# Kernel tuning notes

Hardware: AMD Instinct MI355X
Metric: run time of the kernel (lower is better)

## Reference

```python
import jax, jax.numpy as jnp
import numpy as np

N, D, F, H, DH, R = 50000, 16, 256, 8, 32, 20
HOP_NUM, TOP_K, ALPHA, NEG_SLOPE = 10, 5, 0.1, 0.2
FF_HID = 4 * F


def _ln(x, g, b, eps=1e-5):
    m = x.mean(-1, keepdims=True)
    v = ((x - m) ** 2).mean(-1, keepdims=True)
    return (x - m) / jnp.sqrt(v + eps) * g + b


def setup_inputs() -> dict:
    key = jax.random.key(0)
    ks = jax.random.split(key, 16)
    s = 0.02
    inp = {
        'ent_feat': jax.random.normal(ks[0], (N, F), jnp.float32),
        'rel_feat': jax.random.normal(ks[1], (R, F), jnp.float32),
        'W_head': jax.random.normal(ks[2], (F, H * DH), jnp.float32) * s,
        'W_tail': jax.random.normal(ks[3], (F, H * DH), jnp.float32) * s,
        'W_ent': jax.random.normal(ks[4], (F, H * DH), jnp.float32) * s,
        'W_rel': jax.random.normal(ks[5], (F, H * DH), jnp.float32) * s,
        'attn_h': jax.random.normal(ks[6], (H, DH), jnp.float32) * s,
        'attn_t': jax.random.normal(ks[7], (H, DH), jnp.float32) * s,
        'attn_r': jax.random.normal(ks[8], (H, DH), jnp.float32) * s,
        'ln_ent_g': jnp.ones((F,), jnp.float32), 'ln_ent_b': jnp.zeros((F,), jnp.float32),
        'ln_rel_g': jnp.ones((F,), jnp.float32), 'ln_rel_b': jnp.zeros((F,), jnp.float32),
        'ln_ff_g': jnp.ones((F,), jnp.float32), 'ln_ff_b': jnp.zeros((F,), jnp.float32),
        'ffn_W1': jax.random.normal(ks[9], (F, FF_HID), jnp.float32) * s,
        'ffn_b1': jnp.zeros((FF_HID,), jnp.float32),
        'ffn_W2': jax.random.normal(ks[10], (FF_HID, F), jnp.float32) * s,
        'ffn_b2': jnp.zeros((F,), jnp.float32),
        'src': jax.random.randint(ks[11], (N, D), 0, N, jnp.int32),
        'rid': jax.random.randint(ks[12], (N, D), 0, R, jnp.int32),
    }
    return inp


def reference(ent_feat, rel_feat, W_head, W_tail, W_ent, W_rel,
              attn_h, attn_t, attn_r,
              ln_ent_g, ln_ent_b, ln_rel_g, ln_rel_b, ln_ff_g, ln_ff_b,
              ffn_W1, ffn_b1, ffn_W2, ffn_b2, src, rid):
    # --- projections (dropout = 0 at eval) ---
    x = _ln(ent_feat, ln_ent_g, ln_ent_b)                    # [N,F]
    fh = (x @ W_head).reshape(N, H, DH)
    ftl = (x @ W_tail).reshape(N, H, DH)
    fe = (x @ W_ent).reshape(N, H, DH)                       # 'ft' messages
    r = _ln(rel_feat, ln_rel_g, ln_rel_b)
    fr = (r @ W_rel).reshape(R, H, DH)
    # --- per-node / per-relation attention logits ---
    eh = (fh * attn_h).sum(-1)                               # [N,H]
    et = (ftl * attn_t).sum(-1)                              # [N,H]
    er = (fr * attn_r).sum(-1)                               # [R,H]
    # edges: row i = incoming edges of dst node i, sources src[i,:]
    e = eh[src] + et[:, None, :] + er[rid]                   # [N,D,H]
    e = jnp.where(e > 0, e, NEG_SLOPE * e)                   # LeakyReLU
    # --- edge_softmax over incoming edges of each dst node ---
    a = jax.nn.softmax(e, axis=1)                            # [N,D,H]
    # --- top-k sparsification + renormalization ---
    a_t = a.transpose(0, 2, 1)                               # [N,H,D]
    topv, _ = jax.lax.top_k(a_t, TOP_K)                      # [N,H,K]
    kth = topv[..., TOP_K - 1]                               # [N,H]
    top_sum = topv.sum(-1)                                   # [N,H]
    a_n = jnp.where(a_t >= kth[..., None], a_t, 0.0) / top_sum[..., None]  # [N,H,D]
    # --- PPR diffusion: feat <- (1-a) * A @ feat + a * feat0 ---
    feat0 = fe

    def step(feat, _):
        m = feat[src]                                        # [N,D,H,DH]
        agg = jnp.einsum('ndhk,nhd->nhk', m, a_n)            # [N,H,DH]
        return (1.0 - ALPHA) * agg + ALPHA * feat0, None

    feat, _ = jax.lax.scan(step, feat0, None, length=HOP_NUM)
    # --- residual (Identity since in==out) + FFN block ---
    rst = feat + ent_feat.reshape(N, H, DH)
    rst = rst.reshape(N, F)
    y = _ln(rst, ln_ff_g, ln_ff_b)
    ff = jax.nn.relu(y @ ffn_W1 + ffn_b1) @ ffn_W2 + ffn_b2
    return ff + rst
```

## Files before the change

kernel.cpp:

```cpp
#include <hip/hip_runtime.h>

#define NN   50000
#define DD   16
#define FFE  256
#define HH   8
#define DHH  32
#define RR   20
#define HOPN 10

typedef unsigned short u16;
typedef unsigned int   u32;
typedef __attribute__((ext_vector_type(8))) short  short8;
typedef __attribute__((ext_vector_type(4))) float  floatx4;

__device__ __forceinline__ float b2f(u16 u){ return __uint_as_float(((u32)u)<<16); }
__device__ __forceinline__ u16 f2b(float f){
  u32 x = __float_as_uint(f);
  u32 r = (x + 0x7fffu + ((x>>16)&1u)) >> 16;
  return (u16)r;
}

__global__ __launch_bounds__(256) void castw_kernel(
    const float* __restrict__ We, const float* __restrict__ W1,
    const float* __restrict__ W2,
    u16* __restrict__ Wet, u16* __restrict__ W1t, u16* __restrict__ W2t)
{
  int tid = blockIdx.x*256 + threadIdx.x;
  if (tid < 256*256) {
    int k = tid >> 8, n = tid & 255;
    Wet[n*256 + k] = f2b(We[tid]);
  } else if (tid < 256*256 + 256*1024) {
    int s = tid - 65536;
    int k = s >> 10, n = s & 1023;
    W1t[n*256 + k] = f2b(W1[s]);
  } else if (tid < 589824) {
    int s = tid - 327680;
    int k = s >> 8, n = s & 255;
    W2t[n*1024 + k] = f2b(W2[s]);
  }
}

__global__ __launch_bounds__(256) void prep_kernel(
    const float* __restrict__ rel_feat,
    const float* __restrict__ W_head, const float* __restrict__ W_tail,
    const float* __restrict__ W_rel,
    const float* __restrict__ attn_h, const float* __restrict__ attn_t,
    const float* __restrict__ attn_r,
    const float* __restrict__ lng, const float* __restrict__ lnb,
    double* __restrict__ Wc, double* __restrict__ er)
{
  int t = threadIdx.x;
  if (blockIdx.x == RR) {
    for (int h = 0; h < HH; h++) {
      double sh = 0.0, st = 0.0;
      #pragma unroll
      for (int c = 0; c < DHH; c++) {
        int j = h*DHH + c;
        sh += (double)W_head[t*FFE + j] * (double)attn_h[j];
        st += (double)W_tail[t*FFE + j] * (double)attn_t[j];
      }
      Wc[t*16 + h]     = sh;
      Wc[t*16 + 8 + h] = st;
    }
    return;
  }
  int r = blockIdx.x;
  __shared__ double red[8];
  __shared__ double rln[256];
  double v = (double)rel_feat[r*FFE + t];
  double s = v, q = v*v;
  #pragma unroll
  for (int o = 32; o; o >>= 1) { s += __shfl_xor(s, o, 64); q += __shfl_xor(q, o, 64); }
  if ((t & 63) == 0) { red[t>>6] = s; red[4 + (t>>6)] = q; }
  __syncthreads();
  double stot = red[0]+red[1]+red[2]+red[3];
  double qtot = red[4]+red[5]+red[6]+red[7];
  double mean = stot * (1.0/256.0);
  double var  = qtot * (1.0/256.0) - mean*mean;
  double rstd = 1.0 / sqrt(var + 1e-5);
  rln[t] = (v - mean) * rstd * (double)lng[t] + (double)lnb[t];
  __syncthreads();
  double acc = 0.0;
  for (int k = 0; k < 256; k++) acc += rln[k] * (double)W_rel[k*FFE + t];
  double p = acc * (double)attn_r[t];
  #pragma unroll
  for (int o = 16; o; o >>= 1) p += __shfl_down(p, o, 32);
  if ((t & 31) == 0) er[r*HH + (t>>5)] = p;
}

__global__ __launch_bounds__(256) void logits_kernel(
    const float* __restrict__ ent,
    const float* __restrict__ lng, const float* __restrict__ lnb,
    const double* __restrict__ Wc,
    u16* __restrict__ xb, double* __restrict__ eh, double* __restrict__ et)
{
  int tid = threadIdx.x;
  int w = tid >> 6, l = tid & 63;
  int rowA = blockIdx.x*8 + w*2;
  int rowB = rowA + 1;
  float gg[4], bbv[4];
  #pragma unroll
  for (int j = 0; j < 4; j++) { gg[j] = lng[l + 64*j]; bbv[j] = lnb[l + 64*j]; }
  double xA[4], xB[4];
  #pragma unroll
  for (int j = 0; j < 4; j++) xA[j] = (double)ent[(size_t)rowA*FFE + l + 64*j];
  #pragma unroll
  for (int j = 0; j < 4; j++) xB[j] = (double)ent[(size_t)rowB*FFE + l + 64*j];
  double sA = xA[0]+xA[1]+xA[2]+xA[3];
  double sB = xB[0]+xB[1]+xB[2]+xB[3];
  double qA = xA[0]*xA[0]+xA[1]*xA[1]+xA[2]*xA[2]+xA[3]*xA[3];
  double qB = xB[0]*xB[0]+xB[1]*xB[1]+xB[2]*xB[2]+xB[3]*xB[3];
  #pragma unroll
  for (int o = 32; o; o >>= 1) {
    sA += __shfl_xor(sA, o, 64); qA += __shfl_xor(qA, o, 64);
    sB += __shfl_xor(sB, o, 64); qB += __shfl_xor(qB, o, 64);
  }
  double mA = sA * (1.0/256.0), mB = sB * (1.0/256.0);
  double vA = qA * (1.0/256.0) - mA*mA, vB = qB * (1.0/256.0) - mB*mB;
  double rsA = 1.0 / sqrt(vA + 1e-5), rsB = 1.0 / sqrt(vB + 1e-5);
  #pragma unroll
  for (int j = 0; j < 4; j++) {
    double yA = (xA[j]-mA)*rsA*(double)gg[j] + (double)bbv[j];
    double yB = (xB[j]-mB)*rsB*(double)gg[j] + (double)bbv[j];
    xA[j] = yA; xB[j] = yB;
    xb[(size_t)rowA*FFE + l + 64*j] = f2b((float)yA);
    xb[(size_t)rowB*FFE + l + 64*j] = f2b((float)yB);
  }
  double accA[16], accB[16];
  #pragma unroll
  for (int o = 0; o < 16; o++) { accA[o] = 0.0; accB[o] = 0.0; }
  #pragma unroll
  for (int j = 0; j < 4; j++) {
    int k = l + 64*j;
    const double2* wp = (const double2*)(Wc + (size_t)k*16);
    double wv[16];
    #pragma unroll
    for (int u = 0; u < 8; u++) { double2 tv = wp[u]; wv[2*u] = tv.x; wv[2*u+1] = tv.y; }
    #pragma unroll
    for (int o = 0; o < 16; o++) {
      accA[o] = fma(xA[j], wv[o], accA[o]);
      accB[o] = fma(xB[j], wv[o], accB[o]);
    }
  }
  #pragma unroll
  for (int o = 0; o < 16; o++) {
    #pragma unroll
    for (int off = 32; off; off >>= 1) {
      accA[o] += __shfl_xor(accA[o], off, 64);
      accB[o] += __shfl_xor(accB[o], off, 64);
    }
  }
  #pragma unroll
  for (int o = 0; o < 16; o++) {
    if (l == o) {
      if (o < 8) eh[(size_t)rowA*HH + o] = accA[o];
      else       et[(size_t)rowA*HH + (o-8)] = accA[o];
    }
    if (l == 16 + o) {
      if (o < 8) eh[(size_t)rowB*HH + o] = accB[o];
      else       et[(size_t)rowB*HH + (o-8)] = accB[o];
    }
  }
}

template<int EPI>
__global__ __launch_bounds__(256) void gemm_kernel(
    const u16* __restrict__ A, const u16* __restrict__ B,
    const float* __restrict__ bias,
    const u16* __restrict__ feat, const float* __restrict__ ent,
    u16* __restrict__ Obf, float* __restrict__ Of,
    int M, int N, int K)
{
  __shared__ u16 As[128][40];
  __shared__ u16 Bs[128][40];
  int t = threadIdx.x;
  int i0 = blockIdx.x * 128;
  int n0 = blockIdx.y * 128;
  int w = t >> 6, l = t & 63;
  int cr = t >> 2;
  int cc = (t & 3) * 8;
  int ga0 = min(i0 + cr, M-1);
  int ga1 = min(i0 + cr + 64, M-1);
  int gb0 = n0 + cr;
  int gb1 = n0 + cr + 64;
  floatx4 acc[2][8];
  #pragma unroll
  for (int mt = 0; mt < 2; mt++)
    #pragma unroll
    for (int nt = 0; nt < 8; nt++) acc[mt][nt] = (floatx4){0.f,0.f,0.f,0.f};
  int ln = l & 15, lq = (l >> 4) * 8;
  for (int k0 = 0; k0 < K; k0 += 32) {
    __syncthreads();
    *(uint4*)&As[cr][cc]      = *(const uint4*)&A[(size_t)ga0*K + k0 + cc];
    *(uint4*)&As[cr+64][cc]   = *(const uint4*)&A[(size_t)ga1*K + k0 + cc];
    *(uint4*)&Bs[cr][cc]      = *(const uint4*)&B[(size_t)gb0*K + k0 + cc];
    *(uint4*)&Bs[cr+64][cc]   = *(const uint4*)&B[(size_t)gb1*K + k0 + cc];
    __syncthreads();
    short8 bfr[8];
    #pragma unroll
    for (int nt = 0; nt < 8; nt++) bfr[nt] = *(const short8*)&Bs[nt*16 + ln][lq];
    #pragma unroll
    for (int mt = 0; mt < 2; mt++) {
      short8 afr = *(const short8*)&As[w*32 + mt*16 + ln][lq];
      #pragma unroll
      for (int nt = 0; nt < 8; nt++)
        acc[mt][nt] = __builtin_amdgcn_mfma_f32_16x16x32_bf16(afr, bfr[nt], acc[mt][nt], 0, 0, 0);
    }
  }
  int lr = (l >> 4) * 4;
  #pragma unroll
  for (int mt = 0; mt < 2; mt++) {
    #pragma unroll
    for (int nt = 0; nt < 8; nt++) {
      int col = n0 + nt*16 + ln;
      #pragma unroll
      for (int r = 0; r < 4; r++) {
        int row = i0 + w*32 + mt*16 + lr + r;
        if (row < M) {
          float v = acc[mt][nt][r];
          if (EPI == 0) {
            Obf[(size_t)row*N + col] = f2b(v);
          } else if (EPI == 1) {
            v += bias[col];
            Obf[(size_t)row*N + col] = f2b(v > 0.f ? v : 0.f);
          } else {
            v += bias[col] + b2f(feat[(size_t)row*FFE + col]) + ent[(size_t)row*FFE + col];
            Of[(size_t)row*N + col] = v;
          }
        }
      }
    }
  }
}

__global__ __launch_bounds__(256) void edge_kernel(
    const int* __restrict__ src, const int* __restrict__ rid,
    const double* __restrict__ eh, const double* __restrict__ et,
    const double* __restrict__ er,
    int* __restrict__ idx6, float* __restrict__ w6)
{
  int tid = blockIdx.x*256 + threadIdx.x;
  if (tid >= NN*HH) return;
  int i = tid >> 3, h = tid & 7;
  double bet = et[tid];
  double e[16]; int sj[16];
  #pragma unroll
  for (int d = 0; d < 16; d++) {
    int s = src[i*DD + d];
    int rv = rid[i*DD + d];
    sj[d] = s;
    double v = eh[s*HH + h] + bet + er[rv*HH + h];
    e[d] = (v > 0.0) ? v : 0.2 * v;
  }
  u32 mask = 0; double vs[5]; int js[5];
  #pragma unroll
  for (int k = 0; k < 5; k++) {
    double best = -1e300; int bj = 0, bd = 0;
    #pragma unroll
    for (int d = 0; d < 16; d++) {
      bool c = (((mask>>d)&1u) == 0u) && (e[d] > best);
      if (c) { best = e[d]; bj = sj[d]; bd = d; }
    }
    mask |= (1u << bd); vs[k] = best; js[k] = bj;
  }
  double kth = vs[4];
  int j6 = 0; bool f6 = false;
  #pragma unroll
  for (int d = 0; d < 16; d++) {
    if ((((mask>>d)&1u) == 0u) && (e[d] == kth) && !f6) { j6 = sj[d]; f6 = true; }
  }
  float m0 = (float)vs[0];
  float ex[5], ssum = 0.f;
  #pragma unroll
  for (int k = 0; k < 5; k++) { ex[k] = __expf((float)vs[k] - m0); ssum += ex[k]; }
  float inv = 0.9f / ssum;
  long base = (long)tid * 6;
  #pragma unroll
  for (int k = 0; k < 5; k++) { idx6[base+k] = js[k]; w6[base+k] = ex[k]*inv; }
  idx6[base+5] = j6; w6[base+5] = f6 ? ex[4]*inv : 0.f;
}

__global__ __launch_bounds__(256) void diff_kernel(
    const u16* __restrict__ fold, const u16* __restrict__ fe,
    const int* __restrict__ idx6, const float* __restrict__ w6,
    u16* __restrict__ fnew)
{
  int tid = threadIdx.x;
  int i = blockIdx.x*2 + (tid >> 7);
  int t2 = tid & 127;
  int h = t2 >> 4, c2 = t2 & 15;
  const u32* fold32 = (const u32*)fold;
  const u32* fe32   = (const u32*)fe;
  u32* fnew32 = (u32*)fnew;
  long eb = ((long)i*HH + h) * 6;
  u32 fv = fe32[(size_t)i*128 + t2];
  float acc0 = 0.1f * b2f((u16)(fv & 0xffff));
  float acc1 = 0.1f * b2f((u16)(fv >> 16));
  #pragma unroll
  for (int k = 0; k < 5; k++) {
    int j = idx6[eb + k];
    float w = w6[eb + k];
    u32 v = fold32[(size_t)j*128 + h*16 + c2];
    acc0 += w * b2f((u16)(v & 0xffff));
    acc1 += w * b2f((u16)(v >> 16));
  }
  float w5 = w6[eb + 5];
  if (w5 != 0.f) {
    int j = idx6[eb + 5];
    u32 v = fold32[(size_t)j*128 + h*16 + c2];
    acc0 += w5 * b2f((u16)(v & 0xffff));
    acc1 += w5 * b2f((u16)(v >> 16));
  }
  fnew32[(size_t)i*128 + t2] = (u32)f2b(acc0) | ((u32)f2b(acc1) << 16);
}

__global__ __launch_bounds__(256) void ln_ff_kernel(
    const u16* __restrict__ feat, const float* __restrict__ ent,
    const float* __restrict__ g, const float* __restrict__ b,
    u16* __restrict__ y)
{
  int w = threadIdx.x >> 6, l = threadIdx.x & 63;
  int row = blockIdx.x*4 + w;
  float4 e4 = *(const float4*)&ent[row*FFE + l*4];
  ushort4 fv = *(const ushort4*)&feat[row*FFE + l*4];
  float v0 = b2f(fv.x)+e4.x, v1 = b2f(fv.y)+e4.y;
  float v2 = b2f(fv.z)+e4.z, v3 = b2f(fv.w)+e4.w;
  float s = v0+v1+v2+v3;
  float q = v0*v0 + v1*v1 + v2*v2 + v3*v3;
  #pragma unroll
  for (int o = 32; o; o >>= 1) { s += __shfl_xor(s, o, 64); q += __shfl_xor(q, o, 64); }
  float mean = s * (1.f/256.f);
  float var  = q * (1.f/256.f) - mean*mean;
  float rstd = rsqrtf(var + 1e-5f);
  float4 g4 = *(const float4*)&g[l*4];
  float4 b4 = *(const float4*)&b[l*4];
  ushort4 o4;
  o4.x = f2b((v0-mean)*rstd*g4.x + b4.x);
  o4.y = f2b((v1-mean)*rstd*g4.y + b4.y);
  o4.z = f2b((v2-mean)*rstd*g4.z + b4.z);
  o4.w = f2b((v3-mean)*rstd*g4.w + b4.w);
  *(ushort4*)&y[row*FFE + l*4] = o4;
}

extern "C" void kernel_launch(void* const* d_in, const int* in_sizes, int n_in,
                              void* d_out, int out_size, void* d_ws, size_t ws_size,
                              hipStream_t stream)
{
  const float* ent      = (const float*)d_in[0];
  const float* rel      = (const float*)d_in[1];
  const float* W_head   = (const float*)d_in[2];
  const float* W_tail   = (const float*)d_in[3];
  const float* W_ent    = (const float*)d_in[4];
  const float* W_rel    = (const float*)d_in[5];
  const float* attn_h   = (const float*)d_in[6];
  const float* attn_t   = (const float*)d_in[7];
  const float* attn_r   = (const float*)d_in[8];
  const float* ln_ent_g = (const float*)d_in[9];
  const float* ln_ent_b = (const float*)d_in[10];
  const float* ln_rel_g = (const float*)d_in[11];
  const float* ln_rel_b = (const float*)d_in[12];
  const float* ln_ff_g  = (const float*)d_in[13];
  const float* ln_ff_b  = (const float*)d_in[14];
  const float* W1       = (const float*)d_in[15];
  const float* b1       = (const float*)d_in[16];
  const float* W2       = (const float*)d_in[17];
  const float* b2       = (const float*)d_in[18];
  const int* src        = (const int*)d_in[19];
  const int* rid        = (const int*)d_in[20];
  float* out = (float*)d_out;

  char* w = (char*)d_ws;
  double* er64 = (double*)(w + 0);
  double* Wc   = (double*)(w + 4096);
  double* eh64 = (double*)(w + 36864);
  double* et64 = (double*)(w + 3236864);
  u16*    xb   = (u16*)  (w + 6436864);
  u16*    fe   = (u16*)  (w + 32036864);
  u16*    fA   = (u16*)  (w + 57636864);
  int*    idx6 = (int*)  (w + 83236864);
  float*  w6   = (float*)(w + 92836864);
  u16*    h1   = (u16*)  (w + 0);
  u16*    fB   = (u16*)  (w + 102436864);
  u16*    y    = (u16*)  (w + 128036864);
  u16*    Wet  = (u16*)  (w + 153636864);
  u16*    W1t  = (u16*)  (w + 153767936);
  u16*    W2t  = (u16*)  (w + 154292224);

  castw_kernel<<<2304, 256, 0, stream>>>(W_ent, W1, W2, Wet, W1t, W2t);
  prep_kernel<<<RR+1, 256, 0, stream>>>(rel, W_head, W_tail, W_rel,
                                        attn_h, attn_t, attn_r,
                                        ln_rel_g, ln_rel_b, Wc, er64);
  logits_kernel<<<NN/8, 256, 0, stream>>>(ent, ln_ent_g, ln_ent_b, Wc,
                                          xb, eh64, et64);
  {
    dim3 g((NN + 127)/128, 2);
    gemm_kernel<0><<<g, 256, 0, stream>>>(xb, Wet, nullptr, nullptr, nullptr,
                                          fe, nullptr, NN, 256, 256);
  }
  edge_kernel<<<(NN*HH + 255)/256, 256, 0, stream>>>(src, rid, eh64, et64, er64,
                                                     idx6, w6);
  const u16* cur = fe;
  u16* bufs[2] = { fA, fB };
  for (int hop = 0; hop < HOPN; hop++) {
    u16* nxt = bufs[hop & 1];
    diff_kernel<<<NN/2, 256, 0, stream>>>(cur, fe, idx6, w6, nxt);
    cur = nxt;
  }
  ln_ff_kernel<<<NN/4, 256, 0, stream>>>(cur, ent, ln_ff_g, ln_ff_b, y);
  {
    dim3 g((NN + 127)/128, 8);
    gemm_kernel<1><<<g, 256, 0, stream>>>(y, W1t, b1, nullptr, nullptr,
                                          h1, nullptr, NN, 1024, 256);
  }
  {
    dim3 g((NN + 127)/128, 2);
    gemm_kernel<2><<<g, 256, 0, stream>>>(h1, W2t, b2, cur, ent,
                                          nullptr, out, NN, 256, 1024);
  }
}
```

Before: 891.3 us.

## Pack edge records and widen diffusion gathers to 16-byte loads

```diff
diff --git a/kernel.cpp b/kernel.cpp
--- a/kernel.cpp
+++ b/kernel.cpp
@@ -19,6 +19,8 @@
   u32 r = (x + 0x7fffu + ((x>>16)&1u)) >> 16;
   return (u16)r;
 }
+__device__ __forceinline__ float blo(u32 u){ return __uint_as_float(u << 16); }
+__device__ __forceinline__ float bhi(u32 u){ return __uint_as_float(u & 0xffff0000u); }
 
 __global__ __launch_bounds__(256) void castw_kernel(
     const float* __restrict__ We, const float* __restrict__ W1,
@@ -142,24 +144,52 @@
       accB[o] = fma(xB[j], wv[o], accB[o]);
     }
   }
-  #pragma unroll
-  for (int o = 0; o < 16; o++) {
-    #pragma unroll
-    for (int off = 32; off; off >>= 1) {
-      accA[o] += __shfl_xor(accA[o], off, 64);
-      accB[o] += __shfl_xor(accB[o], off, 64);
-    }
-  }
-  #pragma unroll
-  for (int o = 0; o < 16; o++) {
-    if (l == o) {
-      if (o < 8) eh[(size_t)rowA*HH + o] = accA[o];
-      else       et[(size_t)rowA*HH + (o-8)] = accA[o];
-    }
-    if (l == 16 + o) {
-      if (o < 8) eh[(size_t)rowB*HH + o] = accB[o];
-      else       et[(size_t)rowB*HH + (o-8)] = accB[o];
-    }
+  int b0 = l & 1, b1 = (l>>1)&1, b2 = (l>>2)&1, b3 = (l>>3)&1;
+  double r1A[8], r1B[8];
+  #pragma unroll
+  for (int s = 0; s < 8; s++) {
+    double kA = b0 ? accA[8+s] : accA[s];
+    double dA = b0 ? accA[s]   : accA[8+s];
+    double kB = b0 ? accB[8+s] : accB[s];
+    double dB = b0 ? accB[s]   : accB[8+s];
+    r1A[s] = kA + __shfl_xor(dA, 1, 64);
+    r1B[s] = kB + __shfl_xor(dB, 1, 64);
+  }
+  double r2A[4], r2B[4];
+  #pragma unroll
+  for (int s = 0; s < 4; s++) {
+    double kA = b1 ? r1A[4+s] : r1A[s];
+    double dA = b1 ? r1A[s]   : r1A[4+s];
+    double kB = b1 ? r1B[4+s] : r1B[s];
+    double dB = b1 ? r1B[s]   : r1B[4+s];
+    r2A[s] = kA + __shfl_xor(dA, 2, 64);
+    r2B[s] = kB + __shfl_xor(dB, 2, 64);
+  }
+  double r3A[2], r3B[2];
+  #pragma unroll
+  for (int s = 0; s < 2; s++) {
+    double kA = b2 ? r2A[2+s] : r2A[s];
+    double dA = b2 ? r2A[s]   : r2A[2+s];
+    double kB = b2 ? r2B[2+s] : r2B[s];
+    double dB = b2 ? r2B[s]   : r2B[2+s];
+    r3A[s] = kA + __shfl_xor(dA, 4, 64);
+    r3B[s] = kB + __shfl_xor(dB, 4, 64);
+  }
+  double k4A = b3 ? r3A[1] : r3A[0];
+  double d4A = b3 ? r3A[0] : r3A[1];
+  double k4B = b3 ? r3B[1] : r3B[0];
+  double d4B = b3 ? r3B[0] : r3B[1];
+  double fA4 = k4A + __shfl_xor(d4A, 8, 64);
+  double fB4 = k4B + __shfl_xor(d4B, 8, 64);
+  fA4 += __shfl_xor(fA4, 16, 64);  fB4 += __shfl_xor(fB4, 16, 64);
+  fA4 += __shfl_xor(fA4, 32, 64);  fB4 += __shfl_xor(fB4, 32, 64);
+  int o = (b0<<3) | (b1<<2) | (b2<<1) | b3;
+  if (l < 16) {
+    if (o < 8) eh[(size_t)rowA*HH + o] = fA4;
+    else       et[(size_t)rowA*HH + (o-8)] = fA4;
+  } else if (l < 32) {
+    if (o < 8) eh[(size_t)rowB*HH + o] = fB4;
+    else       et[(size_t)rowB*HH + (o-8)] = fB4;
   }
 }
 
@@ -237,7 +267,7 @@
     const int* __restrict__ src, const int* __restrict__ rid,
     const double* __restrict__ eh, const double* __restrict__ et,
     const double* __restrict__ er,
-    int* __restrict__ idx6, float* __restrict__ w6)
+    uint4* __restrict__ rec)
 {
   int tid = blockIdx.x*256 + threadIdx.x;
   if (tid >= NN*HH) return;
@@ -274,44 +304,62 @@
   #pragma unroll
   for (int k = 0; k < 5; k++) { ex[k] = __expf((float)vs[k] - m0); ssum += ex[k]; }
   float inv = 0.9f / ssum;
-  long base = (long)tid * 6;
-  #pragma unroll
-  for (int k = 0; k < 5; k++) { idx6[base+k] = js[k]; w6[base+k] = ex[k]*inv; }
-  idx6[base+5] = j6; w6[base+5] = f6 ? ex[4]*inv : 0.f;
+  float w5 = f6 ? ex[4]*inv : 0.f;
+  size_t rb = (size_t)tid * 4;
+  rec[rb+0] = make_uint4((u32)js[0], (u32)js[1], (u32)js[2], (u32)js[3]);
+  rec[rb+1] = make_uint4((u32)js[4], (u32)j6,
+                         __float_as_uint(ex[0]*inv), __float_as_uint(ex[1]*inv));
+  rec[rb+2] = make_uint4(__float_as_uint(ex[2]*inv), __float_as_uint(ex[3]*inv),
+                         __float_as_uint(ex[4]*inv), __float_as_uint(w5));
 }
 
 __global__ __launch_bounds__(256) void diff_kernel(
     const u16* __restrict__ fold, const u16* __restrict__ fe,
-    const int* __restrict__ idx6, const float* __restrict__ w6,
-    u16* __restrict__ fnew)
+    const uint4* __restrict__ rec, u16* __restrict__ fnew)
 {
   int tid = threadIdx.x;
-  int i = blockIdx.x*2 + (tid >> 7);
-  int t2 = tid & 127;
-  int h = t2 >> 4, c2 = t2 & 15;
-  const u32* fold32 = (const u32*)fold;
-  const u32* fe32   = (const u32*)fe;
-  u32* fnew32 = (u32*)fnew;
-  long eb = ((long)i*HH + h) * 6;
-  u32 fv = fe32[(size_t)i*128 + t2];
-  float acc0 = 0.1f * b2f((u16)(fv & 0xffff));
-  float acc1 = 0.1f * b2f((u16)(fv >> 16));
+  int g = tid >> 2, q = tid & 3;
+  int i = blockIdx.x*8 + (g >> 3);
+  int h = g & 7;
+  const uint4* f4  = (const uint4*)fold;
+  const uint4* fe4 = (const uint4*)fe;
+  uint4* fn4 = (uint4*)fnew;
+  size_t rb = ((size_t)i*HH + h) * 4;
+  uint4 ra = rec[rb], rbv = rec[rb+1], rc = rec[rb+2];
+  int idx[6] = {(int)ra.x,(int)ra.y,(int)ra.z,(int)ra.w,(int)rbv.x,(int)rbv.y};
+  float wv[6];
+  wv[0]=__uint_as_float(rbv.z); wv[1]=__uint_as_float(rbv.w);
+  wv[2]=__uint_as_float(rc.x);  wv[3]=__uint_as_float(rc.y);
+  wv[4]=__uint_as_float(rc.z);  wv[5]=__uint_as_float(rc.w);
+  int co = h*4 + q;
+  uint4 fv = fe4[(size_t)i*32 + co];
+  float a0 = 0.1f*blo(fv.x), a1 = 0.1f*bhi(fv.x);
+  float a2 = 0.1f*blo(fv.y), a3 = 0.1f*bhi(fv.y);
+  float a4 = 0.1f*blo(fv.z), a5 = 0.1f*bhi(fv.z);
+  float a6 = 0.1f*blo(fv.w), a7 = 0.1f*bhi(fv.w);
   #pragma unroll
   for (int k = 0; k < 5; k++) {
-    int j = idx6[eb + k];
-    float w = w6[eb + k];
-    u32 v = fold32[(size_t)j*128 + h*16 + c2];
-    acc0 += w * b2f((u16)(v & 0xffff));
-    acc1 += w * b2f((u16)(v >> 16));
-  }
-  float w5 = w6[eb + 5];
-  if (w5 != 0.f) {
-    int j = idx6[eb + 5];
-    u32 v = fold32[(size_t)j*128 + h*16 + c2];
-    acc0 += w5 * b2f((u16)(v & 0xffff));
-    acc1 += w5 * b2f((u16)(v >> 16));
-  }
-  fnew32[(size_t)i*128 + t2] = (u32)f2b(acc0) | ((u32)f2b(acc1) << 16);
+    uint4 v = f4[(size_t)idx[k]*32 + co];
+    float wk = wv[k];
+    a0 += wk*blo(v.x); a1 += wk*bhi(v.x);
+    a2 += wk*blo(v.y); a3 += wk*bhi(v.y);
+    a4 += wk*blo(v.z); a5 += wk*bhi(v.z);
+    a6 += wk*blo(v.w); a7 += wk*bhi(v.w);
+  }
+  if (wv[5] != 0.f) {
+    uint4 v = f4[(size_t)idx[5]*32 + co];
+    float wk = wv[5];
+    a0 += wk*blo(v.x); a1 += wk*bhi(v.x);
+    a2 += wk*blo(v.y); a3 += wk*bhi(v.y);
+    a4 += wk*blo(v.z); a5 += wk*bhi(v.z);
+    a6 += wk*blo(v.w); a7 += wk*bhi(v.w);
+  }
+  uint4 o;
+  o.x = (u32)f2b(a0) | ((u32)f2b(a1) << 16);
+  o.y = (u32)f2b(a2) | ((u32)f2b(a3) << 16);
+  o.z = (u32)f2b(a4) | ((u32)f2b(a5) << 16);
+  o.w = (u32)f2b(a6) | ((u32)f2b(a7) << 16);
+  fn4[(size_t)i*32 + co] = o;
 }
 
 __global__ __launch_bounds__(256) void ln_ff_kernel(
@@ -375,10 +423,9 @@
   double* eh64 = (double*)(w + 36864);
   double* et64 = (double*)(w + 3236864);
   u16*    xb   = (u16*)  (w + 6436864);
+  uint4*  rec  = (uint4*)(w + 6436864);
   u16*    fe   = (u16*)  (w + 32036864);
   u16*    fA   = (u16*)  (w + 57636864);
-  int*    idx6 = (int*)  (w + 83236864);
-  float*  w6   = (float*)(w + 92836864);
   u16*    h1   = (u16*)  (w + 0);
   u16*    fB   = (u16*)  (w + 102436864);
   u16*    y    = (u16*)  (w + 128036864);
@@ -398,12 +445,12 @@
                                           fe, nullptr, NN, 256, 256);
   }
   edge_kernel<<<(NN*HH + 255)/256, 256, 0, stream>>>(src, rid, eh64, et64, er64,
-                                                     idx6, w6);
+                                                     rec);
   const u16* cur = fe;
   u16* bufs[2] = { fA, fB };
   for (int hop = 0; hop < HOPN; hop++) {
     u16* nxt = bufs[hop & 1];
-    diff_kernel<<<NN/2, 256, 0, stream>>>(cur, fe, idx6, w6, nxt);
+    diff_kernel<<<NN/8, 256, 0, stream>>>(cur, fe, rec, nxt);
     cur = nxt;
   }
   ln_ff_kernel<<<NN/4, 256, 0, stream>>>(cur, ent, ln_ff_g, ln_ff_b, y);
```

Measured after the change: 896.8 us. About the same (+0.6%).
